# Optimization experiments

Measured on AMD Instinct MI355X. Metric: run time of the kernel, lower is better.

## Reference

```python
import jax, jax.numpy as jnp
import numpy as np

# dims
N, T = 16, 2000            # batch, encoder frames
ENC, DEC = 512, 512        # enc_dim, dec_dim
ATT, C, K, H = 512, 10, 64, 4  # att_dim, conv_channels, loc_context, att_head


def setup_inputs() -> dict:
    key = jax.random.key(0)
    ks = jax.random.split(key, 16)
    s = 0.02
    enc_pad = jax.random.normal(ks[0], (N, T, ENC), jnp.float32)
    enc_len = jax.random.randint(ks[1], (N,), T // 2, T + 1, jnp.int32)
    dec_prev = jax.random.normal(ks[2], (N, DEC), jnp.float32)
    ali_prev = jax.random.uniform(ks[3], (N, H, T), jnp.float32)
    ali_prev = ali_prev / ali_prev.sum(-1, keepdims=True)
    # parameters (torch layout)
    We = jax.random.normal(ks[4], (ATT * H, ENC), jnp.float32) * s   # enc_proj weight
    be = jnp.zeros((ATT * H,), jnp.float32)                          # enc_proj bias
    Wk = jax.random.normal(ks[5], (ATT * H, ENC), jnp.float32) * s   # key_proj
    Wd = jax.random.normal(ks[6], (ATT * H, DEC), jnp.float32) * s   # dec_proj
    WF = jax.random.normal(ks[7], (C * H, 1, 2 * K + 1), jnp.float32) * s  # F: grouped conv1d
    bF = jnp.zeros((C * H,), jnp.float32)
    Wa = jax.random.normal(ks[8], (H, ATT, C), jnp.float32) * s      # att: 1x1 grouped conv, per-head [ATT,C]
    Ww = jax.random.normal(ks[9], (H, ATT), jnp.float32) * s         # w: 1x1 grouped conv, per-head [ATT]
    Wc = jax.random.normal(ks[10], (ENC, ATT * H), jnp.float32) * s  # ctx_proj
    bc = jnp.zeros((ENC,), jnp.float32)
    return {"enc_pad": enc_pad, "enc_len": enc_len, "dec_prev": dec_prev,
            "ali_prev": ali_prev, "We": We, "be": be, "Wk": Wk, "Wd": Wd,
            "WF": WF, "bF": bF, "Wa": Wa, "Ww": Ww, "Wc": Wc, "bc": bc}


def reference(enc_pad, enc_len, dec_prev, ali_prev, We, be, Wk, Wd, WF, bF, Wa, Ww, Wc, bc):
    n, t, _ = enc_pad.shape
    # enc_part: N x H x T x D
    ep = enc_pad @ We.T + be
    enc_part = ep.reshape(n, t, H, ATT).transpose(0, 2, 1, 3)
    # key_part: N x H x D x T (matches torch transpose(1,2).view ordering)
    kp = enc_pad @ Wk.T
    key_part = kp.transpose(0, 2, 1).reshape(n, H, ATT, t)
    # pad mask: N x T, True where padded
    pad_mask = jnp.arange(t)[None, :] >= enc_len[:, None]
    # location features: grouped conv1d over alignment, per head
    f = jax.lax.conv_general_dilated(
        ali_prev, WF, window_strides=(1,), padding=[(K, K)],
        dimension_numbers=("NCH", "OIH", "NCH"), feature_group_count=H)
    f = (f + bF[None, :, None]).reshape(n, H, C, t)
    # 1x1 grouped conv: C -> ATT per head
    att_part = jnp.einsum("hdc,nhct->nhdt", Wa, f)
    dec_part = (dec_prev @ Wd.T).reshape(n, H, ATT)
    sum_part = jnp.tanh(att_part + key_part + dec_part[..., None])  # N x H x D x T
    score = jnp.einsum("hd,nhdt->nht", Ww, sum_part)                # N x H x T
    score = jnp.where(pad_mask[:, None, :], -jnp.inf, score)
    ali = jax.nn.softmax(score, axis=-1)
    ctx = jnp.einsum("nht,nhtd->nhd", ali, enc_part).reshape(n, H * ATT)
    ctx = ctx @ Wc.T + bc
    return ali, ctx
```

## Files before the change

### kernel.cpp

```cpp
#include <hip/hip_runtime.h>

#define NB   16
#define TT   2000
#define TP   2048
#define SPT  2048
#define ENC  512
#define ATTD 512
#define HH   4
#define CC   10
#define KK   64
#define KW   129
#define HATT 2048

typedef unsigned short u16;
typedef __attribute__((ext_vector_type(8))) short bf16x8;
typedef __attribute__((ext_vector_type(4))) float f32x4;

#define AS1 __attribute__((address_space(1)))
#define AS3 __attribute__((address_space(3)))

#define CVT_BLOCKS   2176
#define CVT_THREADS  (CVT_BLOCKS * 256)

__device__ inline unsigned bfpack2(float lo, float hi) {
    unsigned a = __builtin_bit_cast(unsigned, lo);
    unsigned b = __builtin_bit_cast(unsigned, hi);
    a = (a + 0x7fffu + ((a >> 16) & 1u)) >> 16;
    b = (b + 0x7fffu + ((b >> 16) & 1u)) >> 16;
    return a | (b << 16);
}

__global__ __launch_bounds__(256) void prep_kernel(
    const float* __restrict__ enc, const float* __restrict__ Wk,
    const float* __restrict__ ali_prev, const float* __restrict__ WF,
    const float* __restrict__ bF, const float* __restrict__ dec_prev,
    const float* __restrict__ Wd, const float* __restrict__ Wa,
    const int* __restrict__ enc_len,
    u16* __restrict__ Abf, u16* __restrict__ Wkbf,
    u16* __restrict__ ftb, u16* __restrict__ wab,
    float* __restrict__ decp)
{
    __shared__ union {
        struct { float aliW[632]; float wfT[KW * CC]; float bfs[CC]; } cv;
        float dsl[16 * 128];
    } sm;
    const int bid = blockIdx.x, tid = threadIdx.x;

    if (bid < CVT_BLOCKS) {
        const long long ATOT = (long long)NB * TP * ENC;
        #pragma unroll
        for (int it = 0; it < 4; it++) {
            long long cid = (long long)it * CVT_THREADS + bid * 256 + tid;
            long long gid = cid * 8;
            if (gid < ATOT) {
                int n = (int)(gid >> 20);
                int rem = (int)(gid & ((1 << 20) - 1));
                int r = rem >> 9, e = rem & 511;
                if (r < enc_len[n]) {
                    const float* s = enc + ((long long)n * TT + r) * ENC + e;
                    float4 v0 = *(const float4*)s;
                    float4 v1 = *(const float4*)(s + 4);
                    uint4 out;
                    out.x = bfpack2(v0.x, v0.y); out.y = bfpack2(v0.z, v0.w);
                    out.z = bfpack2(v1.x, v1.y); out.w = bfpack2(v1.z, v1.w);
                    *(uint4*)(Abf + gid) = out;
                }
            } else {
                long long j = gid - ATOT;
                const float* s = Wk + j;
                float4 v0 = *(const float4*)s;
                float4 v1 = *(const float4*)(s + 4);
                uint4 out;
                out.x = bfpack2(v0.x, v0.y); out.y = bfpack2(v0.z, v0.w);
                out.z = bfpack2(v1.x, v1.y); out.w = bfpack2(v1.z, v1.w);
                *(uint4*)(Wkbf + j) = out;
            }
        }
    } else if (bid < CVT_BLOCKS + 256) {
        int b2 = bid - CVT_BLOCKS;
        int tc = b2 & 3, h = (b2 >> 2) & 3, n = b2 >> 4;
        int t0 = tc * 500;
        float* aliW = sm.cv.aliW;
        float* wfT  = sm.cv.wfT;
        float* bfs  = sm.cv.bfs;
        const float* arow = ali_prev + ((long long)n * HH + h) * TT;
        for (int i = tid; i < 632; i += 256) {
            int tt = t0 - KK + i;
            aliW[i] = (tt >= 0 && tt < TT) ? arow[tt] : 0.f;
        }
        for (int i = tid; i < KW * CC; i += 256) {
            int k = i / CC, c = i - k * CC;
            wfT[i] = WF[(h * CC + c) * KW + k];
        }
        if (tid < CC) bfs[tid] = bF[h * CC + tid];
        __syncthreads();
        if (tid < 250) {
            float acc0[CC], acc1[CC];
            #pragma unroll
            for (int c = 0; c < CC; c++) { acc0[c] = 0.f; acc1[c] = 0.f; }
            const int base = 2 * tid;
            float2 w0 = *(const float2*)&aliW[base];
            for (int k = 0; k < 128; k += 2) {
                float2 w2 = *(const float2*)&aliW[base + k + 2];
                #pragma unroll
                for (int cj = 0; cj < 5; cj++) {
                    float2 fk  = *(const float2*)&wfT[k * CC + cj * 2];
                    float2 fk1 = *(const float2*)&wfT[(k + 1) * CC + cj * 2];
                    acc0[2*cj]   += w0.x * fk.x + w0.y * fk1.x;
                    acc0[2*cj+1] += w0.x * fk.y + w0.y * fk1.y;
                    acc1[2*cj]   += w0.y * fk.x + w2.x * fk1.x;
                    acc1[2*cj+1] += w0.y * fk.y + w2.x * fk1.y;
                }
                w0 = w2;
            }
            #pragma unroll
            for (int cj = 0; cj < 5; cj++) {
                float2 fk = *(const float2*)&wfT[128 * CC + cj * 2];
                acc0[2*cj]   += w0.x * fk.x;  acc0[2*cj+1] += w0.x * fk.y;
                acc1[2*cj]   += w0.y * fk.x;  acc1[2*cj+1] += w0.y * fk.y;
            }
            #pragma unroll
            for (int c = 0; c < CC; c++) { acc0[c] += bfs[c]; acc1[c] += bfs[c]; }
            int t = t0 + base;
            u16* frow = ftb + (((long long)(n * HH + h)) * TP + t) * 16;
            uint4 ra, rb;
            ra.x = bfpack2(acc0[0], acc0[1]); ra.y = bfpack2(acc0[2], acc0[3]);
            ra.z = bfpack2(acc0[4], acc0[5]); ra.w = bfpack2(acc0[6], acc0[7]);
            rb.x = bfpack2(acc0[8], acc0[9]); rb.y = 0u; rb.z = 0u; rb.w = 0u;
            *(uint4*)(frow)     = ra; *(uint4*)(frow + 8)  = rb;
            ra.x = bfpack2(acc1[0], acc1[1]); ra.y = bfpack2(acc1[2], acc1[3]);
            ra.z = bfpack2(acc1[4], acc1[5]); ra.w = bfpack2(acc1[6], acc1[7]);
            rb.x = bfpack2(acc1[8], acc1[9]);
            *(uint4*)(frow + 16) = ra; *(uint4*)(frow + 24) = rb;
        } else if (tc == 3) {
            uint4 z = {0u, 0u, 0u, 0u};
            int r0 = 2000 + (tid - 250) * 8;
            u16* frow = ftb + (((long long)(n * HH + h)) * TP + r0) * 16;
            for (int r = 0; r < 8; r++) {
                *(uint4*)(frow + r * 16)     = z;
                *(uint4*)(frow + r * 16 + 8) = z;
            }
        }
    } else if (bid < CVT_BLOCKS + 288) {
        int b2 = bid - (CVT_BLOCKS + 256);
        int kc = b2 >> 3, jc = b2 & 7;
        for (int i = tid; i < 2048; i += 256) {
            int nn = i >> 7, kk = i & 127;
            sm.dsl[i] = dec_prev[nn * 512 + kc * 128 + kk];
        }
        __syncthreads();
        int d = jc * 256 + tid;
        float acc[NB];
        #pragma unroll
        for (int n = 0; n < NB; n++) acc[n] = 0.f;
        const float4* w4 = (const float4*)(Wd + (long long)d * 512 + kc * 128);
        for (int e4 = 0; e4 < 32; e4++) {
            float4 w = w4[e4];
            #pragma unroll
            for (int n = 0; n < NB; n++) {
                const float* a = sm.dsl + n * 128 + e4 * 4;
                acc[n] += w.x * a[0] + w.y * a[1] + w.z * a[2] + w.w * a[3];
            }
        }
        #pragma unroll
        for (int n = 0; n < NB; n++) decp[((long long)kc * NB + n) * HATT + d] = acc[n];
    } else {
        int b2 = bid - (CVT_BLOCKS + 288);
        int j0 = b2 * 512 + tid * 2;
        #pragma unroll
        for (int q = 0; q < 2; q++) {
            int j = j0 + q;
            int hh = j >> 9, dd = j & 511;
            const float* wr = Wa + ((long long)(hh * ATTD + dd)) * CC;
            uint4 ra, rb;
            ra.x = bfpack2(wr[0], wr[1]); ra.y = bfpack2(wr[2], wr[3]);
            ra.z = bfpack2(wr[4], wr[5]); ra.w = bfpack2(wr[6], wr[7]);
            rb.x = bfpack2(wr[8], wr[9]); rb.y = 0u; rb.z = 0u; rb.w = 0u;
            u16* out = wab + (long long)j * 16;
            *(uint4*)(out)     = ra;
            *(uint4*)(out + 8) = rb;
        }
    }
}

__global__ __launch_bounds__(256, 4) void score_gemm_kernel(
    const u16* __restrict__ Abf, const u16* __restrict__ Bbf,
    const u16* __restrict__ ftb, const u16* __restrict__ wab,
    const float* __restrict__ decp, const float* __restrict__ Ww,
    const int* __restrict__ enc_len, float* __restrict__ score_part)
{
    __shared__ __attribute__((aligned(16))) char smem[32768];
    float* sred = (float*)smem;

    const int bid = blockIdx.x;
    const int xcd = bid & 7;
    const int lcl = bid >> 3;
    const int nt = lcl & 15;
    const int rr = lcl >> 4;
    const int n = rr >> 1, half = rr & 1;
    const int mtl = (xcd + n) & 7;
    const int mt = half ? (8 + mtl) : mtl;

    if (mt * 128 >= enc_len[n]) return;

    const int tid = threadIdx.x, wave = tid >> 6, lane = tid & 63;
    const int l16 = lane & 15, lk = lane >> 4;
    const int h = nt >> 2;

    const u16* Aptr = Abf + ((long long)n * TP + mt * 128) * ENC;
    const u16* Bptr = Bbf + (long long)nt * 128 * ENC;

    f32x4 acc[4][4];
    #pragma unroll
    for (int mi = 0; mi < 4; mi++)
        #pragma unroll
        for (int nj = 0; nj < 4; nj++) {
            f32x4 z = {0.f, 0.f, 0.f, 0.f};
            acc[mi][nj] = z;
        }

    const int wrow = (wave >> 1) * 64, wcol = (wave & 1) * 64;
    const int t0 = mt * 128, dd0 = (nt & 3) * 128;

    for (int kt = 0; kt < 8; kt++) {
        const int k0 = kt * 64;
        #pragma unroll
        for (int i = 0; i < 4; i++) {
            int b = i * 4096 + tid * 16;
            int r = b >> 7, kb = b & 127;
            int kbs = kb ^ ((r & 7) << 4);
            __builtin_amdgcn_global_load_lds(
                (const AS1 void*)(Aptr + r * ENC + k0 + (kbs >> 1)),
                (AS3 void*)(smem + i * 4096 + wave * 1024), 16, 0, 0);
            __builtin_amdgcn_global_load_lds(
                (const AS1 void*)(Bptr + r * ENC + k0 + (kbs >> 1)),
                (AS3 void*)(smem + 16384 + i * 4096 + wave * 1024), 16, 0, 0);
        }
        __syncthreads();
        #pragma unroll
        for (int ks = 0; ks < 64; ks += 32) {
            bf16x8 af[4], bf[4];
            #pragma unroll
            for (int mi = 0; mi < 4; mi++) {
                int row = wrow + mi * 16 + l16;
                int cb = (ks * 2 + lk * 16) ^ ((row & 7) << 4);
                af[mi] = *(const bf16x8*)(smem + row * 128 + cb);
            }
            #pragma unroll
            for (int nj = 0; nj < 4; nj++) {
                int row = wcol + nj * 16 + l16;
                int cb = (ks * 2 + lk * 16) ^ ((row & 7) << 4);
                bf[nj] = *(const bf16x8*)(smem + 16384 + row * 128 + cb);
            }
            #pragma unroll
            for (int mi = 0; mi < 4; mi++)
                #pragma unroll
                for (int nj = 0; nj < 4; nj++)
                    acc[mi][nj] = __builtin_amdgcn_mfma_f32_16x16x32_bf16(
                        af[mi], bf[nj], acc[mi][nj], 0, 0, 0);
        }
        __syncthreads();
    }

    {
        bf16x8 zer = {0, 0, 0, 0, 0, 0, 0, 0};
        bf16x8 af[4], bf[4];
        #pragma unroll
        for (int mi = 0; mi < 4; mi++) af[mi] = zer;
        #pragma unroll
        for (int nj = 0; nj < 4; nj++) bf[nj] = zer;
        if (lk < 2) {
            #pragma unroll
            for (int mi = 0; mi < 4; mi++)
                af[mi] = *(const bf16x8*)(ftb +
                    (((long long)(n * HH + h)) * TP + t0 + wrow + mi * 16 + l16) * 16 + lk * 8);
            #pragma unroll
            for (int nj = 0; nj < 4; nj++)
                bf[nj] = *(const bf16x8*)(wab +
                    ((long long)(nt * 128 + wcol + nj * 16 + l16)) * 16 + lk * 8);
        }
        #pragma unroll
        for (int mi = 0; mi < 4; mi++)
            #pragma unroll
            for (int nj = 0; nj < 4; nj++)
                acc[mi][nj] = __builtin_amdgcn_mfma_f32_16x16x32_bf16(
                    af[mi], bf[nj], acc[mi][nj], 0, 0, 0);
    }

    float wm2[4], dec4[4];
    #pragma unroll
    for (int nj = 0; nj < 4; nj++) {
        int cl = wcol + nj * 16 + l16;
        wm2[nj] = -2.f * Ww[h * ATTD + dd0 + cl];
        int j = nt * 128 + cl;
        dec4[nj] = decp[((long long)0 * NB + n) * HATT + j]
                 + decp[((long long)1 * NB + n) * HATT + j]
                 + decp[((long long)2 * NB + n) * HATT + j]
                 + decp[((long long)3 * NB + n) * HATT + j];
    }

    #pragma unroll
    for (int mi = 0; mi < 4; mi++) {
        #pragma unroll
        for (int j = 0; j < 4; j++) {
            int rl = wrow + mi * 16 + lk * 4 + j;
            float s = 0.f;
            #pragma unroll
            for (int nj = 0; nj < 4; nj++) {
                float v = acc[mi][nj][j] + dec4[nj];
                float e = __expf(v + v);
                s = fmaf(wm2[nj], __builtin_amdgcn_rcpf(e + 1.f), s);
            }
            s += __shfl_xor(s, 1); s += __shfl_xor(s, 2);
            s += __shfl_xor(s, 4); s += __shfl_xor(s, 8);
            if (l16 == 0) sred[(wave & 1) * 128 + rl] = s;
        }
    }
    __syncthreads();
    if (tid < 128) {
        int t = t0 + tid;
        if (t < TT)
            score_part[((long long)((nt & 3) * NB + n) * HH + h) * SPT + t] =
                sred[tid] + sred[128 + tid];
    }
}

__global__ __launch_bounds__(256) void softmax_kernel(
    const float* __restrict__ score_part, const int* __restrict__ enc_len,
    float* __restrict__ ali)
{
    int n = blockIdx.x >> 2, h = blockIdx.x & 3;
    int len = enc_len[n];
    int tid = threadIdx.x;
    int t0 = tid * 8;
    float s[8];
    #pragma unroll
    for (int i = 0; i < 8; i++) s[i] = 0.f;
    #pragma unroll
    for (int q = 0; q < 4; q++) {
        const float* rb = score_part + (((long long)(q * NB + n)) * HH + h) * SPT + t0;
        float4 a = *(const float4*)rb;
        float4 b = *(const float4*)(rb + 4);
        s[0] += a.x; s[1] += a.y; s[2] += a.z; s[3] += a.w;
        s[4] += b.x; s[5] += b.y; s[6] += b.z; s[7] += b.w;
    }
    float lmax = -3.4e38f;
    #pragma unroll
    for (int i = 0; i < 8; i++) {
        if (t0 + i < len) lmax = fmaxf(lmax, s[i]);
    }
    __shared__ float red[256];
    red[tid] = lmax; __syncthreads();
    for (int off = 128; off; off >>= 1) {
        if (tid < off) red[tid] = fmaxf(red[tid], red[tid + off]);
        __syncthreads();
    }
    float bmax = red[0];
    __syncthreads();
    float lsum = 0.f;
    #pragma unroll
    for (int i = 0; i < 8; i++) {
        if (t0 + i < len) { s[i] = expf(s[i] - bmax); lsum += s[i]; }
        else s[i] = 0.f;
    }
    red[tid] = lsum; __syncthreads();
    for (int off = 128; off; off >>= 1) {
        if (tid < off) red[tid] += red[tid + off];
        __syncthreads();
    }
    float inv = 1.f / red[0];
    float* arow = ali + ((long long)n * HH + h) * TT;
    if (t0 + 8 <= TT) {
        float4 o0 = {s[0] * inv, s[1] * inv, s[2] * inv, s[3] * inv};
        float4 o1 = {s[4] * inv, s[5] * inv, s[6] * inv, s[7] * inv};
        *(float4*)(arow + t0) = o0;
        *(float4*)(arow + t0 + 4) = o1;
    } else {
        for (int i = 0; i < 8; i++)
            if (t0 + i < TT) arow[t0 + i] = s[i] * inv;
    }
}

__global__ __launch_bounds__(256) void a_enc_kernel(
    const float* __restrict__ ali, const u16* __restrict__ Abf,
    const int* __restrict__ enc_len, float* __restrict__ aep)
{
    int tc = blockIdx.x & 31, n = blockIdx.x >> 5;
    int tid = threadIdx.x;
    int len = enc_len[n];
    int tbeg = tc * 63;
    int cnt = len - tbeg; if (cnt > 63) cnt = 63; if (cnt < 0) cnt = 0;
    __shared__ float aliS[HH][64];
    __shared__ float red[2][4][129];
    {
        int hh = tid >> 6, tt = tid & 63;
        aliS[hh][tt] = (tt < cnt) ? ali[((long long)n * HH + hh) * TT + tbeg + tt] : 0.f;
    }
    __syncthreads();
    const int l = tid & 127, tq = tid >> 7;
    float acc[HH][4];
    #pragma unroll
    for (int hh = 0; hh < HH; hh++)
        #pragma unroll
        for (int k = 0; k < 4; k++) acc[hh][k] = 0.f;
    #pragma unroll 4
    for (int ii = 0; ii < 32; ii++) {
        int tl = ii * 2 + tq;
        if (tl < cnt) {
            uint2 u = *(const uint2*)(Abf + ((long long)n * TP + tbeg + tl) * ENC + l * 4);
            float e0 = __builtin_bit_cast(float, u.x << 16);
            float e1 = __builtin_bit_cast(float, u.x & 0xffff0000u);
            float e2 = __builtin_bit_cast(float, u.y << 16);
            float e3 = __builtin_bit_cast(float, u.y & 0xffff0000u);
            #pragma unroll
            for (int hh = 0; hh < HH; hh++) {
                float w = aliS[hh][tl];
                acc[hh][0] += w * e0; acc[hh][1] += w * e1;
                acc[hh][2] += w * e2; acc[hh][3] += w * e3;
            }
        }
    }
    #pragma unroll
    for (int hh = 0; hh < HH; hh++) {
        __syncthreads();
        #pragma unroll
        for (int k = 0; k < 4; k++) red[tq][k][l] = acc[hh][k];
        __syncthreads();
        int d2 = tid * 2;
        float v0 = red[0][d2 & 3][d2 >> 2] + red[1][d2 & 3][d2 >> 2];
        int d3 = d2 + 1;
        float v1 = red[0][d3 & 3][d3 >> 2] + red[1][d3 & 3][d3 >> 2];
        float2 o = {v0, v1};
        *(float2*)(aep + (((long long)tc * NB + n) * HH + hh) * ENC + d2) = o;
    }
}

__global__ __launch_bounds__(256) void ctx_tmp_kernel(
    const float* __restrict__ aep, const float* __restrict__ We,
    const float* __restrict__ be, float* __restrict__ ctmp)
{
    int kc = blockIdx.x >> 4, jc = blockIdx.x & 15;
    int tid = threadIdx.x;
    int h = (jc * 128) >> 9;
    __shared__ float aes[16 * 64];
    for (int i = tid; i < 1024; i += 256) {
        int nn = i >> 6, kk = i & 63;
        float s = 0.f;
        for (int tc = 0; tc < 32; tc++)
            s += aep[(((long long)tc * NB + nn) * HH + h) * ENC + kc * 64 + kk];
        aes[i] = s;
    }
    __syncthreads();
    int j = jc * 128 + (tid & 127);
    int nh = tid >> 7;
    float acc[8];
    #pragma unroll
    for (int n2 = 0; n2 < 8; n2++) acc[n2] = 0.f;
    const float4* w4 = (const float4*)(We + (long long)j * 512 + kc * 64);
    for (int e4 = 0; e4 < 16; e4++) {
        float4 w = w4[e4];
        #pragma unroll
        for (int n2 = 0; n2 < 8; n2++) {
            const float* a = aes + (nh * 8 + n2) * 64 + e4 * 4;
            acc[n2] += w.x * a[0] + w.y * a[1] + w.z * a[2] + w.w * a[3];
        }
    }
    float bias = (kc == 0) ? be[j] : 0.f;
    #pragma unroll
    for (int n2 = 0; n2 < 8; n2++)
        ctmp[((long long)kc * NB + nh * 8 + n2) * HATT + j] = acc[n2] + bias;
}

__global__ __launch_bounds__(256) void ctx_out_kernel(
    const float* __restrict__ ctmp, const float* __restrict__ Wc,
    const float* __restrict__ bc, float* __restrict__ out_ctx)
{
    int ec = blockIdx.x & 15, nc = blockIdx.x >> 4;
    int tid = threadIdx.x;
    __shared__ float ct[4 * 2048];
    __shared__ float red[8][4][33];
    for (int i = tid; i < 4 * 2048; i += 256) {
        int nn = i >> 11, j = i & 2047;
        int n = nc * 4 + nn;
        float s = 0.f;
        #pragma unroll
        for (int kc = 0; kc < 8; kc++)
            s += ctmp[((long long)kc * NB + n) * HATT + j];
        ct[i] = s;
    }
    __syncthreads();
    int eo = tid & 31, kq = tid >> 5;
    int eg = ec * 32 + eo;
    float acc[4];
    #pragma unroll
    for (int nn = 0; nn < 4; nn++) acc[nn] = 0.f;
    const float4* w4 = (const float4*)(Wc + (long long)eg * HATT + kq * 256);
    for (int j4 = 0; j4 < 64; j4++) {
        float4 w = w4[j4];
        #pragma unroll
        for (int nn = 0; nn < 4; nn++) {
            const float* a = ct + nn * 2048 + kq * 256 + j4 * 4;
            acc[nn] += w.x * a[0] + w.y * a[1] + w.z * a[2] + w.w * a[3];
        }
    }
    #pragma unroll
    for (int nn = 0; nn < 4; nn++) red[kq][nn][eo] = acc[nn];
    __syncthreads();
    if (tid < 128) {
        int eo2 = tid & 31, nn2 = tid >> 5;
        float s = 0.f;
        #pragma unroll
        for (int kq2 = 0; kq2 < 8; kq2++) s += red[kq2][nn2][eo2];
        out_ctx[((long long)(nc * 4 + nn2)) * 512 + ec * 32 + eo2] = s + bc[ec * 32 + eo2];
    }
}

extern "C" void kernel_launch(void* const* d_in, const int* in_sizes, int n_in,
                              void* d_out, int out_size, void* d_ws, size_t ws_size,
                              hipStream_t stream)
{
    (void)in_sizes; (void)n_in; (void)out_size; (void)ws_size;
    const float* enc_pad  = (const float*)d_in[0];
    const int*   enc_len  = (const int*)  d_in[1];
    const float* dec_prev = (const float*)d_in[2];
    const float* ali_prev = (const float*)d_in[3];
    const float* We = (const float*)d_in[4];
    const float* be = (const float*)d_in[5];
    const float* Wk = (const float*)d_in[6];
    const float* Wd = (const float*)d_in[7];
    const float* WF = (const float*)d_in[8];
    const float* bF = (const float*)d_in[9];
    const float* Wa = (const float*)d_in[10];
    const float* Ww = (const float*)d_in[11];
    const float* Wc = (const float*)d_in[12];
    const float* bc = (const float*)d_in[13];

    char* ws = (char*)d_ws;
    u16*   Abf  = (u16*)  (ws);
    u16*   Wkbf = (u16*)  (ws + 33554432);
    u16*   ftb  = (u16*)  (ws + 35651584);
    u16*   wab  = (u16*)  (ws + 39845888);
    float* decp = (float*)(ws + 39911424);
    float* spart= (float*)(ws + 40435712);
    float* aep  = (float*)(ws + 40435712);
    float* ctmp = (float*)(ws + 35651584);

    float* ali = (float*)d_out;
    float* ctx = (float*)d_out + NB * HH * TT;

    prep_kernel      <<<2468, 256, 0, stream>>>(enc_pad, Wk, ali_prev, WF, bF,
                                                dec_prev, Wd, Wa, enc_len,
                                                Abf, Wkbf, ftb, wab, decp);
    score_gemm_kernel<<<4096, 256, 0, stream>>>(Abf, Wkbf, ftb, wab, decp, Ww,
                                                enc_len, spart);
    softmax_kernel   <<<64,   256, 0, stream>>>(spart, enc_len, ali);
    a_enc_kernel     <<<512,  256, 0, stream>>>(ali, Abf, enc_len, aep);
    ctx_tmp_kernel   <<<128,  256, 0, stream>>>(aep, We, be, ctmp);
    ctx_out_kernel   <<<64,   256, 0, stream>>>(ctmp, Wc, bc, ctx);
}
```

Before: 169.6 us.

## Split softmax into partial max/sum stats and fuse normalization into a_enc

Replaces the 64-block softmax kernel with a 256-block kernel that computes per-quarter max and sum-of-exponentials. The a_enc kernel then combines the four partial statistics, recomputes normalized alignment values straight from the score partials, and writes ali itself. This raises parallelism in the reduction stage and removes the separate ali round trip. In exchange, each a_enc block redundantly recomputes the global statistics and the exponentials, and workspace buffers are reassigned.

```diff
diff --git a/kernel.cpp b/kernel.cpp
--- a/kernel.cpp
+++ b/kernel.cpp
@@ -325,30 +325,25 @@
     }
 }
 
-__global__ __launch_bounds__(256) void softmax_kernel(
+__global__ __launch_bounds__(256) void smax_part_kernel(
     const float* __restrict__ score_part, const int* __restrict__ enc_len,
-    float* __restrict__ ali)
-{
-    int n = blockIdx.x >> 2, h = blockIdx.x & 3;
+    float* __restrict__ mstat)
+{
+    int qr = blockIdx.x & 3, h = (blockIdx.x >> 2) & 3, n = blockIdx.x >> 4;
     int len = enc_len[n];
     int tid = threadIdx.x;
-    int t0 = tid * 8;
-    float s[8];
-    #pragma unroll
-    for (int i = 0; i < 8; i++) s[i] = 0.f;
+    int t = qr * 512 + tid * 2;
+    float s0 = 0.f, s1 = 0.f;
     #pragma unroll
     for (int q = 0; q < 4; q++) {
-        const float* rb = score_part + (((long long)(q * NB + n)) * HH + h) * SPT + t0;
-        float4 a = *(const float4*)rb;
-        float4 b = *(const float4*)(rb + 4);
-        s[0] += a.x; s[1] += a.y; s[2] += a.z; s[3] += a.w;
-        s[4] += b.x; s[5] += b.y; s[6] += b.z; s[7] += b.w;
-    }
+        float2 sv = *(const float2*)(score_part +
+            (((long long)(q * NB + n)) * HH + h) * SPT + t);
+        s0 += sv.x; s1 += sv.y;
+    }
+    bool v0 = (t < len), v1 = (t + 1 < len);
     float lmax = -3.4e38f;
-    #pragma unroll
-    for (int i = 0; i < 8; i++) {
-        if (t0 + i < len) lmax = fmaxf(lmax, s[i]);
-    }
+    if (v0) lmax = s0;
+    if (v1) lmax = fmaxf(lmax, s1);
     __shared__ float red[256];
     red[tid] = lmax; __syncthreads();
     for (int off = 128; off; off >>= 1) {
@@ -358,32 +353,23 @@
     float bmax = red[0];
     __syncthreads();
     float lsum = 0.f;
-    #pragma unroll
-    for (int i = 0; i < 8; i++) {
-        if (t0 + i < len) { s[i] = expf(s[i] - bmax); lsum += s[i]; }
-        else s[i] = 0.f;
-    }
+    if (v0) lsum += expf(s0 - bmax);
+    if (v1) lsum += expf(s1 - bmax);
     red[tid] = lsum; __syncthreads();
     for (int off = 128; off; off >>= 1) {
         if (tid < off) red[tid] += red[tid + off];
         __syncthreads();
     }
-    float inv = 1.f / red[0];
-    float* arow = ali + ((long long)n * HH + h) * TT;
-    if (t0 + 8 <= TT) {
-        float4 o0 = {s[0] * inv, s[1] * inv, s[2] * inv, s[3] * inv};
-        float4 o1 = {s[4] * inv, s[5] * inv, s[6] * inv, s[7] * inv};
-        *(float4*)(arow + t0) = o0;
-        *(float4*)(arow + t0 + 4) = o1;
-    } else {
-        for (int i = 0; i < 8; i++)
-            if (t0 + i < TT) arow[t0 + i] = s[i] * inv;
+    if (tid == 0) {
+        float2 o = {bmax, red[0]};
+        *(float2*)(mstat + ((n * HH + h) * 4 + qr) * 2) = o;
     }
 }
 
 __global__ __launch_bounds__(256) void a_enc_kernel(
-    const float* __restrict__ ali, const u16* __restrict__ Abf,
-    const int* __restrict__ enc_len, float* __restrict__ aep)
+    const float* __restrict__ score_part, const float* __restrict__ mstat,
+    const u16* __restrict__ Abf, const int* __restrict__ enc_len,
+    float* __restrict__ aep, float* __restrict__ ali)
 {
     int tc = blockIdx.x & 31, n = blockIdx.x >> 5;
     int tid = threadIdx.x;
@@ -394,7 +380,24 @@
     __shared__ float red[2][4][129];
     {
         int hh = tid >> 6, tt = tid & 63;
-        aliS[hh][tt] = (tt < cnt) ? ali[((long long)n * HH + hh) * TT + tbeg + tt] : 0.f;
+        int t = tbeg + tt;
+        const float2* ms = (const float2*)(mstat) + (n * HH + hh) * 4;
+        float2 p0 = ms[0], p1 = ms[1], p2 = ms[2], p3 = ms[3];
+        float gm = fmaxf(fmaxf(p0.x, p1.x), fmaxf(p2.x, p3.x));
+        float gs = p0.y * expf(p0.x - gm) + p1.y * expf(p1.x - gm)
+                 + p2.y * expf(p2.x - gm) + p3.y * expf(p3.x - gm);
+        float gi = 1.f / gs;
+        float av = 0.f;
+        if (tt < cnt) {
+            float s = 0.f;
+            #pragma unroll
+            for (int q = 0; q < 4; q++)
+                s += score_part[(((long long)(q * NB + n)) * HH + hh) * SPT + t];
+            av = expf(s - gm) * gi;
+        }
+        aliS[hh][tt] = av;
+        if (tt < 63 && t < TT)
+            ali[((long long)n * HH + hh) * TT + t] = av;
     }
     __syncthreads();
     const int l = tid & 127, tq = tid >> 7;
@@ -542,8 +545,9 @@
     u16*   wab  = (u16*)  (ws + 39845888);
     float* decp = (float*)(ws + 39911424);
     float* spart= (float*)(ws + 40435712);
-    float* aep  = (float*)(ws + 40435712);
-    float* ctmp = (float*)(ws + 35651584);
+    float* aep  = (float*)(ws + 35651584);
+    float* mstat= (float*)(ws + 39845888);
+    float* ctmp = (float*)(ws + 40435712);
 
     float* ali = (float*)d_out;
     float* ctx = (float*)d_out + NB * HH * TT;
@@ -553,8 +557,9 @@
                                                 Abf, Wkbf, ftb, wab, decp);
     score_gemm_kernel<<<4096, 256, 0, stream>>>(Abf, Wkbf, ftb, wab, decp, Ww,
                                                 enc_len, spart);
-    softmax_kernel   <<<64,   256, 0, stream>>>(spart, enc_len, ali);
-    a_enc_kernel     <<<512,  256, 0, stream>>>(ali, Abf, enc_len, aep);
+    smax_part_kernel <<<256,  256, 0, stream>>>(spart, enc_len, mstat);
+    a_enc_kernel     <<<512,  256, 0, stream>>>(spart, mstat, Abf, enc_len,
+                                                aep, ali);
     ctx_tmp_kernel   <<<128,  256, 0, stream>>>(aep, We, be, ctmp);
     ctx_out_kernel   <<<64,   256, 0, stream>>>(ctmp, Wc, bc, ctx);
 }
```

New measurement: 170.1 us. No clear change (+0.3%).
